# Optimization experiments

Measured on AMD Instinct MI355X. Metric: run time of the kernel, lower is better.

The kernel has to match this reference:

```python
import jax, jax.numpy as jnp
import numpy as np

KERNEL = (9, 9, 9)  # box-filter window
KSIZE = KERNEL[0] * KERNEL[1] * KERNEL[2]  # 729
GAMMA = 1.0


def _box_sum(x):
    # x: [B, C, D, H, W] -> channel-sum then 9x9x9 sliding-window sum (SAME pad),
    # exactly matching F.conv3d with an all-ones [1, C, 9,9,9] kernel, pad=4.
    s = jnp.sum(x, axis=1, keepdims=True)  # [B,1,D,H,W]
    return jax.lax.reduce_window(
        s, jnp.asarray(0.0, s.dtype), jax.lax.add,
        window_dimensions=(1, 1) + KERNEL,
        window_strides=(1, 1, 1, 1, 1),
        padding='SAME')


def setup_inputs() -> dict:
    key = jax.random.key(0)
    k1, k2, k3 = jax.random.split(key, 3)
    shape = (2, 1, 160, 160, 160)
    return {
        'input': jax.random.normal(k1, shape, dtype=jnp.float32),
        'target': jax.random.normal(k2, shape, dtype=jnp.float32),
        'flow': jax.random.normal(k3, shape, dtype=jnp.float32),
    }


def reference(input, target, flow):
    # normalize target from (-1, 1) to (0, 1)
    target = (target + 1.0) * 0.5
    w = jax.nn.sigmoid(flow) ** GAMMA  # voxel-wise confidence weight

    T_sum = _box_sum(target)
    I_sum = _box_sum(input)
    TT_sum = _box_sum(target * target)
    II_sum = _box_sum(input * input)
    IT_sum = _box_sum(input * target)

    Ihat = I_sum / KSIZE
    That = T_sum / KSIZE
    cross = IT_sum - Ihat * T_sum - That * I_sum + That * Ihat * KSIZE
    T_var = TT_sum - 2.0 * That * T_sum + That * That * KSIZE
    I_var = II_sum - 2.0 * Ihat * I_sum + Ihat * Ihat * KSIZE

    cc = cross * cross * w / (T_var * I_var + 1e-5)
    return -1.0 * jnp.mean(cc)
```

## Files before the change

### kernel.cpp

```cpp
#include <hip/hip_runtime.h>


constexpr int NB = 2;
constexpr int ND = 160;
constexpr int NH = 160;
constexpr int NW = 160;
constexpr int TH = 16;
constexpr int TW = 16;
constexpr int DCHUNK = 16;
constexpr int NDCH = ND / DCHUNK;
constexpr int NPL = DCHUNK + 8;
constexpr int FS5 = 392;
constexpr int PFS = 264;
constexpr float INV_K = 1.0f / 729.0f;
constexpr double INV_COUNT = 1.0 / (double(NB) * ND * NH * NW);

__device__ __forceinline__ void issue_load(
    const float* __restrict__ in, const float* __restrict__ tg,
    int b, int dp, int h0, int w0, int tid,
    float4& iv, float4& tv)
{
    iv = make_float4(0.f, 0.f, 0.f, 0.f);
    tv = make_float4(0.f, 0.f, 0.f, 0.f);
    if (tid < 144 && ((unsigned)dp < (unsigned)ND)) {
        int r = tid / 6;
        int q = tid - r * 6;
        int gh = h0 - 4 + r;
        int gw = w0 - 4 + q * 4;
        if (((unsigned)gh < (unsigned)NH) && ((unsigned)gw < (unsigned)NW)) {
            int base = ((b * ND + dp) * NH + gh) * NW + gw;
            iv = *reinterpret_cast<const float4*>(in + base);
            float4 rv = *reinterpret_cast<const float4*>(tg + base);
            tv.x = fmaf(rv.x, 0.5f, 0.5f);
            tv.y = fmaf(rv.y, 0.5f, 0.5f);
            tv.z = fmaf(rv.z, 0.5f, 0.5f);
            tv.w = fmaf(rv.w, 0.5f, 0.5f);
        }
    }
}

__device__ __forceinline__ void stage(int tid, const float4& iv, const float4& tv,
                                      float* __restrict__ inT, float* __restrict__ tgT)
{
    if (tid < 144) {
        reinterpret_cast<float4*>(inT)[tid] = iv;
        reinterpret_cast<float4*>(tgT)[tid] = tv;
    }
}

__device__ __forceinline__ void step2(int tid, const float* __restrict__ inT,
                                      const float* __restrict__ tgT,
                                      float* __restrict__ tmp5)
{
    int pos = tid;
    #pragma unroll
    for (int rep = 0; rep < 2; ++rep) {
        if (pos < 384) {
            int r = pos >> 4, wo = pos & 15;
            const float* ir = inT + r * 24 + wo;
            const float* tr = tgT + r * 24 + wo;
            float s0 = 0.f, s1 = 0.f, s2 = 0.f, s3 = 0.f, s4 = 0.f;
            #pragma unroll
            for (int k = 0; k < 9; ++k) {
                float ivv = ir[k];
                float t = tr[k];
                s0 += t;
                s1 += ivv;
                s2 = fmaf(t, t, s2);
                s3 = fmaf(ivv, ivv, s3);
                s4 = fmaf(ivv, t, s4);
            }
            int o = r * 16 + wo;
            tmp5[0 * FS5 + o] = s0;
            tmp5[1 * FS5 + o] = s1;
            tmp5[2 * FS5 + o] = s2;
            tmp5[3 * FS5 + o] = s3;
            tmp5[4 * FS5 + o] = s4;
        }
        pos += 256;
    }
}

__device__ __forceinline__ void step3(int tid, const float* __restrict__ tmp5,
                                      float* __restrict__ Pbuf)
{
    if (tid < 80) {
        int f = tid >> 4, w = tid & 15;
        const float* basep = tmp5 + f * FS5 + w;
        float s = 0.f;
        #pragma unroll
        for (int r = 0; r < 8; ++r) s += basep[r * 16];
        #pragma unroll
        for (int ho = 0; ho < 16; ++ho) {
            s += basep[(ho + 8) * 16];
            Pbuf[f * PFS + ho * 16 + w] = s;
            s -= basep[ho * 16];
        }
    }
}

__device__ __forceinline__ float cc_value(const float S[5], float flv)
{
    float wgt = 1.0f / (1.0f + __expf(-flv));
    float Ts = S[0], Is = S[1], TTs = S[2], IIs = S[3], ITs = S[4];
    float Ihat = Is * INV_K;
    float That = Ts * INV_K;
    float cross = ITs - Ihat * Ts - That * Is + That * Ihat * 729.0f;
    float T_var = TTs - 2.0f * That * Ts + That * That * 729.0f;
    float I_var = IIs - 2.0f * Ihat * Is + Ihat * Ihat * 729.0f;
    return cross * cross * wgt / (T_var * I_var + 1e-5f);
}

__global__ void __launch_bounds__(256)
cc3d_main(const float* __restrict__ in, const float* __restrict__ tg,
          const float* __restrict__ fl, double* __restrict__ acc_out)
{
    __shared__ float inT[24 * 24];
    __shared__ float tgT[24 * 24];
    __shared__ float tmp5[5 * FS5];
    __shared__ float Pbuf[5 * PFS];
    __shared__ float red[4];

    const int tid = threadIdx.x;
    const int w0 = blockIdx.x * TW;
    const int h0 = blockIdx.y * TH;
    const int bz = blockIdx.z;
    const int b  = bz / NDCH;
    const int d0 = (bz - b * NDCH) * DCHUNK;
    const int hh = tid >> 4, ww = tid & 15;

    float ring[45];
    #pragma unroll
    for (int i = 0; i < 45; ++i) ring[i] = 0.f;
    float S[5] = {0.f, 0.f, 0.f, 0.f, 0.f};
    float acc = 0.f;

    float4 iv, tv;
    issue_load(in, tg, b, d0 - 4, h0, w0, tid, iv, tv);

    #pragma unroll
    for (int l = 0; l < 9; ++l) {
        stage(tid, iv, tv, inT, tgT);
        float4 niv, ntv;
        issue_load(in, tg, b, d0 - 4 + l + 1, h0, w0, tid, niv, ntv);
        float flv = 0.f;
        if (l == 8) {
            int fidx = ((b * ND + d0) * NH + (h0 + hh)) * NW + (w0 + ww);
            flv = fl[fidx];
        }
        __syncthreads();
        step2(tid, inT, tgT, tmp5);
        __syncthreads();
        step3(tid, tmp5, Pbuf);
        __syncthreads();
        if (l < 8) {
            #pragma unroll
            for (int f = 0; f < 5; ++f) {
                float pv = Pbuf[f * PFS + tid];
                ring[f * 9 + l] = pv;
                S[f] += pv;
            }
        } else {
            #pragma unroll
            for (int f = 0; f < 5; ++f) {
                float pn = Pbuf[f * PFS + tid];
                S[f] += pn - ring[f * 9 + 8];
                ring[f * 9 + 8] = pn;
            }
            acc += cc_value(S, flv);
        }
        iv = niv; tv = ntv;
    }

    for (int lb = 9; lb < 27; lb += 9) {
        #pragma unroll
        for (int li = 0; li < 9; ++li) {
            const int l = lb + li;
            if (l < NPL) {
                stage(tid, iv, tv, inT, tgT);
                float4 niv, ntv;
                if (l < NPL - 1) {
                    issue_load(in, tg, b, d0 - 4 + l + 1, h0, w0, tid, niv, ntv);
                } else {
                    niv = make_float4(0.f, 0.f, 0.f, 0.f);
                    ntv = niv;
                }
                int dout = d0 + (l - 8);
                int fidx = ((b * ND + dout) * NH + (h0 + hh)) * NW + (w0 + ww);
                float flv = fl[fidx];
                __syncthreads();
                step2(tid, inT, tgT, tmp5);
                __syncthreads();
                step3(tid, tmp5, Pbuf);
                __syncthreads();
                const int slot = li;
                #pragma unroll
                for (int f = 0; f < 5; ++f) {
                    float pn = Pbuf[f * PFS + tid];
                    S[f] += pn - ring[f * 9 + slot];
                    ring[f * 9 + slot] = pn;
                }
                acc += cc_value(S, flv);
                iv = niv; tv = ntv;
            }
        }
    }

    #pragma unroll
    for (int off = 32; off > 0; off >>= 1) acc += __shfl_down(acc, off);
    if ((tid & 63) == 0) red[tid >> 6] = acc;
    __syncthreads();
    if (tid == 0) {
        double v = (double)red[0] + (double)red[1] + (double)red[2] + (double)red[3];
        atomicAdd(acc_out, v);
    }
}

__global__ void cc3d_finalize(const double* __restrict__ acc, float* __restrict__ out)
{
    out[0] = (float)(-(acc[0] * INV_COUNT));
}

extern "C" void kernel_launch(void* const* d_in, const int* in_sizes, int n_in,
                              void* d_out, int out_size, void* d_ws, size_t ws_size,
                              hipStream_t stream)
{
    const float* in = (const float*)d_in[0];
    const float* tg = (const float*)d_in[1];
    const float* fl = (const float*)d_in[2];
    float* out = (float*)d_out;
    double* acc = (double*)d_ws;

    hipMemsetAsync(d_ws, 0, sizeof(double), stream);

    dim3 grid(NW / TW, NH / TH, NB * NDCH);
    cc3d_main<<<grid, dim3(256), 0, stream>>>(in, tg, fl, acc);
    cc3d_finalize<<<1, 1, 0, stream>>>(acc, out);
}
```

Before: 195.7 us.

## Double depth chunk, fuse H-pass into per-thread sums, skip out-of-range planes

```diff
diff --git a/kernel.cpp b/kernel.cpp
--- a/kernel.cpp
+++ b/kernel.cpp
@@ -7,11 +7,10 @@
 constexpr int NW = 160;
 constexpr int TH = 16;
 constexpr int TW = 16;
-constexpr int DCHUNK = 16;
+constexpr int DCHUNK = 32;
 constexpr int NDCH = ND / DCHUNK;
 constexpr int NPL = DCHUNK + 8;
 constexpr int FS5 = 392;
-constexpr int PFS = 264;
 constexpr float INV_K = 1.0f / 729.0f;
 constexpr double INV_COUNT = 1.0 / (double(NB) * ND * NH * NW);
 
@@ -81,24 +80,6 @@
     }
 }
 
-__device__ __forceinline__ void step3(int tid, const float* __restrict__ tmp5,
-                                      float* __restrict__ Pbuf)
-{
-    if (tid < 80) {
-        int f = tid >> 4, w = tid & 15;
-        const float* basep = tmp5 + f * FS5 + w;
-        float s = 0.f;
-        #pragma unroll
-        for (int r = 0; r < 8; ++r) s += basep[r * 16];
-        #pragma unroll
-        for (int ho = 0; ho < 16; ++ho) {
-            s += basep[(ho + 8) * 16];
-            Pbuf[f * PFS + ho * 16 + w] = s;
-            s -= basep[ho * 16];
-        }
-    }
-}
-
 __device__ __forceinline__ float cc_value(const float S[5], float flv)
 {
     float wgt = 1.0f / (1.0f + __expf(-flv));
@@ -118,7 +99,6 @@
     __shared__ float inT[24 * 24];
     __shared__ float tgT[24 * 24];
     __shared__ float tmp5[5 * FS5];
-    __shared__ float Pbuf[5 * PFS];
     __shared__ float red[4];
 
     const int tid = threadIdx.x;
@@ -138,69 +118,37 @@
     float4 iv, tv;
     issue_load(in, tg, b, d0 - 4, h0, w0, tid, iv, tv);
 
-    #pragma unroll
-    for (int l = 0; l < 9; ++l) {
-        stage(tid, iv, tv, inT, tgT);
-        float4 niv, ntv;
-        issue_load(in, tg, b, d0 - 4 + l + 1, h0, w0, tid, niv, ntv);
-        float flv = 0.f;
-        if (l == 8) {
-            int fidx = ((b * ND + d0) * NH + (h0 + hh)) * NW + (w0 + ww);
-            flv = fl[fidx];
-        }
-        __syncthreads();
-        step2(tid, inT, tgT, tmp5);
-        __syncthreads();
-        step3(tid, tmp5, Pbuf);
-        __syncthreads();
-        if (l < 8) {
-            #pragma unroll
-            for (int f = 0; f < 5; ++f) {
-                float pv = Pbuf[f * PFS + tid];
-                ring[f * 9 + l] = pv;
-                S[f] += pv;
-            }
-        } else {
-            #pragma unroll
-            for (int f = 0; f < 5; ++f) {
-                float pn = Pbuf[f * PFS + tid];
-                S[f] += pn - ring[f * 9 + 8];
-                ring[f * 9 + 8] = pn;
-            }
-            acc += cc_value(S, flv);
-        }
-        iv = niv; tv = ntv;
-    }
-
-    for (int lb = 9; lb < 27; lb += 9) {
+    for (int lb = 0; lb < NPL + 8; lb += 9) {
         #pragma unroll
         for (int li = 0; li < 9; ++li) {
             const int l = lb + li;
             if (l < NPL) {
-                stage(tid, iv, tv, inT, tgT);
+                const int dp = d0 - 4 + l;
+                const bool valid = ((unsigned)dp < (unsigned)ND);
+                if (valid) stage(tid, iv, tv, inT, tgT);
                 float4 niv, ntv;
-                if (l < NPL - 1) {
-                    issue_load(in, tg, b, d0 - 4 + l + 1, h0, w0, tid, niv, ntv);
-                } else {
-                    niv = make_float4(0.f, 0.f, 0.f, 0.f);
-                    ntv = niv;
+                issue_load(in, tg, b, dp + 1, h0, w0, tid, niv, ntv);
+                float flv = 0.f;
+                if (l >= 8) {
+                    int dout = d0 + l - 8;
+                    int fidx = ((b * ND + dout) * NH + (h0 + hh)) * NW + (w0 + ww);
+                    flv = fl[fidx];
                 }
-                int dout = d0 + (l - 8);
-                int fidx = ((b * ND + dout) * NH + (h0 + hh)) * NW + (w0 + ww);
-                float flv = fl[fidx];
                 __syncthreads();
-                step2(tid, inT, tgT, tmp5);
+                if (valid) step2(tid, inT, tgT, tmp5);
                 __syncthreads();
-                step3(tid, tmp5, Pbuf);
-                __syncthreads();
-                const int slot = li;
                 #pragma unroll
                 for (int f = 0; f < 5; ++f) {
-                    float pn = Pbuf[f * PFS + tid];
-                    S[f] += pn - ring[f * 9 + slot];
-                    ring[f * 9 + slot] = pn;
+                    float pn = 0.f;
+                    if (valid) {
+                        const float* bp = tmp5 + f * FS5 + hh * 16 + ww;
+                        #pragma unroll
+                        for (int k = 0; k < 9; ++k) pn += bp[k * 16];
+                    }
+                    S[f] += pn - ring[f * 9 + li];
+                    ring[f * 9 + li] = pn;
                 }
-                acc += cc_value(S, flv);
+                if (l >= 8) acc += cc_value(S, flv);
                 iv = niv; tv = ntv;
             }
         }
```

New measurement: 196.2 us. No clear change (+0.3%).
